# Optimization experiments

Measured on AMD Instinct MI355X. Metric: run time of the kernel, lower is better.

The kernel has to match this reference:

```python
import jax, jax.numpy as jnp
import numpy as np

B, M, H, NH = 64, 512, 1024, 8
HD = H // NH
EPS = 1e-5


def setup_inputs() -> dict:
    key = jax.random.key(0)
    ks = jax.random.split(key, 16)
    def n(k, shape, s=0.02):
        return jax.random.normal(k, shape, dtype=jnp.float32) * s
    z = lambda shape: jnp.zeros(shape, jnp.float32)
    return {
        "x": jax.random.normal(ks[0], (B, M, M), dtype=jnp.float32),
        # 1x1 Conv2d(1->H): weight [H,1,1,1] flattened to [H], plus bias [H]
        "conv_w": n(ks[1], (H,)), "conv_b": n(ks[2], (H,)),
        # MLP: Linear(M->H), ReLU, Linear(H->H); weights stored [in,out]
        "w1": n(ks[3], (M, H)), "b1": z((H,)),
        "w2": n(ks[4], (H, H)), "b2": z((H,)),
        "ln_g": jnp.ones((H,), jnp.float32), "ln_b": z((H,)),
        "wq": n(ks[5], (H, H)), "bq": z((H,)),
        "wk": n(ks[6], (H, H)), "bk": z((H,)),
        "wv": n(ks[7], (H, H)), "bv": z((H,)),
        "wo": n(ks[8], (H, H)), "bo": z((H,)),
        "wp": n(ks[9], (H, H)), "bp": z((H,)),
    }


def reference(x, conv_w, conv_b, w1, b1, w2, b2, ln_g, ln_b,
              wq, bq, wk, bk, wv, bv, wo, bo, wp, bp):
    # RegionConvolution: 1x1 conv over 1 input channel to H channels, then
    # mean over channels. Since mean_c(x*w_c + b_c) = x*mean(w) + mean(b),
    # compute the reduced affine form (identical math, no [B,H,M,M] temp).
    x = x + (x * conv_w.mean() + conv_b.mean())          # residual conv add, [B,M,M]
    # RegionEmbeddingMLP
    x_reg = jnp.maximum(x @ w1 + b1, 0.0) @ w2 + b2      # [B,M,H]
    # LayerNorm
    mu = x_reg.mean(-1, keepdims=True)
    var = ((x_reg - mu) ** 2).mean(-1, keepdims=True)
    x_norm = (x_reg - mu) / jnp.sqrt(var + EPS) * ln_g + ln_b
    # MHSA with multiplicative off-diagonal mask (diagonal scores zeroed)
    def heads(y):
        return y.reshape(B, M, NH, HD).transpose(0, 2, 1, 3)  # [B,NH,M,HD]
    q = heads(x_norm @ wq + bq)
    k = heads(x_norm @ wk + bk)
    v = heads(x_norm @ wv + bv)
    scores = jnp.einsum('bhqd,bhkd->bhqk', q, k) / jnp.sqrt(jnp.float32(HD))
    scores = scores * (1.0 - jnp.eye(M, dtype=scores.dtype))  # zero diagonal
    attn = jax.nn.softmax(scores, axis=-1)
    ctx = jnp.einsum('bhqk,bhkd->bhqd', attn, v)
    ctx = ctx.transpose(0, 2, 1, 3).reshape(B, M, H)
    attn_out = ctx @ wo + bo
    attn_out = attn_out @ wp + bp                        # output_proj
    return attn_out + x_reg                              # residual, [B,M,H]
```

## Files before the change

### kernel.cpp

```cpp
#include <hip/hip_runtime.h>
#include <hip/hip_fp16.h>
#include <cstdint>
#include <cstddef>

typedef _Float16 f16;
typedef _Float16 f16x8 __attribute__((ext_vector_type(8)));
typedef _Float16 f16x4 __attribute__((ext_vector_type(4)));
typedef _Float16 f16x2 __attribute__((ext_vector_type(2)));
typedef float f32x4 __attribute__((ext_vector_type(4)));
typedef unsigned int ui4 __attribute__((ext_vector_type(4)));

#define NB 64
#define SEQ 512
#define HDIM 1024
#define NHEAD 8
#define HD 128
#define MR (NB * SEQ)
#define QK_LD 2048

__device__ __forceinline__ void async_copy16(const f16* g, f16* l) {
  __builtin_amdgcn_global_load_lds(
      (__attribute__((address_space(1))) void*)(void*)const_cast<f16*>(g),
      (__attribute__((address_space(3))) void*)l, 16, 0, 0);
}


__global__ __launch_bounds__(256) void conv_reduce(
    const float* __restrict__ cw, const float* __restrict__ cb,
    float* __restrict__ out2) {
  int t = threadIdx.x;
  float a = 0.f, b = 0.f;
  for (int i = t; i < HDIM; i += 256) { a += cw[i]; b += cb[i]; }
  for (int m = 32; m >= 1; m >>= 1) { a += __shfl_xor(a, m); b += __shfl_xor(b, m); }
  __shared__ float sa[4], sb[4];
  if ((t & 63) == 0) { sa[t >> 6] = a; sb[t >> 6] = b; }
  __syncthreads();
  if (t == 0) {
    out2[0] = (sa[0] + sa[1] + sa[2] + sa[3]) * (1.f / HDIM);
    out2[1] = (sb[0] + sb[1] + sb[2] + sb[3]) * (1.f / HDIM);
  }
}

__global__ __launch_bounds__(256) void prep_x(
    const float* __restrict__ x, const float* __restrict__ cs,
    f16* __restrict__ xh) {
  size_t i = (size_t)blockIdx.x * 256 + threadIdx.x;
  float cw = 1.f + cs[0], cb = cs[1];
  float4 v = ((const float4*)x)[i];
  f16x4 o;
  o[0] = (f16)(v.x * cw + cb);
  o[1] = (f16)(v.y * cw + cb);
  o[2] = (f16)(v.z * cw + cb);
  o[3] = (f16)(v.w * cw + cb);
  ((f16x4*)xh)[i] = o;
}

__global__ __launch_bounds__(256) void concat_bias(
    const float* __restrict__ bq, const float* __restrict__ bk,
    const float* __restrict__ bv, float* __restrict__ dst) {
  int i = blockIdx.x * 256 + threadIdx.x;
  if (i < 1024) dst[i] = bq[i];
  else if (i < 2048) dst[i] = bk[i - 1024];
  else dst[i] = bv[i - 2048];
}

__global__ __launch_bounds__(256) void cast_f16(
    const float* __restrict__ src, f16* __restrict__ dst) {
  size_t i = (size_t)blockIdx.x * 256 + threadIdx.x;
  float4 v = ((const float4*)src)[i];
  f16x4 o;
  o[0] = (f16)v.x; o[1] = (f16)v.y; o[2] = (f16)v.z; o[3] = (f16)v.w;
  ((f16x4*)dst)[i] = o;
}

__global__ __launch_bounds__(256) void fuse_bias_p1(
    const float* __restrict__ bo, const float* __restrict__ wp,
    float* __restrict__ partial) {
  int n = blockIdx.x * 256 + threadIdx.x;
  int jc = blockIdx.y;
  float s = 0.f;
#pragma unroll 8
  for (int j = jc * 128; j < jc * 128 + 128; j++) s += bo[j] * wp[(size_t)j * 1024 + n];
  partial[(size_t)jc * 1024 + n] = s;
}

__global__ __launch_bounds__(256) void fuse_bias_p2(
    const float* __restrict__ partial, const float* __restrict__ bp,
    float* __restrict__ bp2) {
  int n = blockIdx.x * 256 + threadIdx.x;
  float s = bp[n];
#pragma unroll
  for (int jc = 0; jc < 8; jc++) s += partial[(size_t)jc * 1024 + n];
  bp2[n] = s;
}

__global__ __launch_bounds__(256) void transpose_cast(
    const float* __restrict__ src, f16* __restrict__ dst, int K, int N) {
  __shared__ float tile[32][33];
  int tx = threadIdx.x, ty = threadIdx.y;
  int n0 = blockIdx.x * 32, k0 = blockIdx.y * 32;
#pragma unroll
  for (int r = 0; r < 32; r += 8) tile[ty + r][tx] = src[(size_t)(k0 + ty + r) * N + n0 + tx];
  __syncthreads();
#pragma unroll
  for (int r = 0; r < 32; r += 8)
    dst[(size_t)(n0 + ty + r) * K + k0 + tx] = (f16)tile[tx][ty + r];
}

__global__ __launch_bounds__(256) void transpose_cast5(
    const float* s0, const float* s1, const float* s2, const float* s3, const float* s4,
    f16* d0, f16* d1, f16* d2, f16* d3, f16* d4) {
  const float* src; f16* dst;
  switch (blockIdx.z) {
    case 0: src = s0; dst = d0; break;
    case 1: src = s1; dst = d1; break;
    case 2: src = s2; dst = d2; break;
    case 3: src = s3; dst = d3; break;
    default: src = s4; dst = d4; break;
  }
  __shared__ float tile[32][33];
  int tx = threadIdx.x, ty = threadIdx.y;
  int n0 = blockIdx.x * 32, k0 = blockIdx.y * 32;
#pragma unroll
  for (int r = 0; r < 32; r += 8) tile[ty + r][tx] = src[(size_t)(k0 + ty + r) * 1024 + n0 + tx];
  __syncthreads();
#pragma unroll
  for (int r = 0; r < 32; r += 8)
    dst[(size_t)(n0 + ty + r) * 1024 + k0 + tx] = (f16)tile[tx][ty + r];
}

__global__ __launch_bounds__(256) void ln_kernel(
    const f16* __restrict__ xin, const float* __restrict__ g,
    const float* __restrict__ bta, f16* __restrict__ out) {
  int row = blockIdx.x;
  int t = threadIdx.x;
  f16x4 vh = ((const f16x4*)(xin + (size_t)row * HDIM))[t];
  float vx = (float)vh[0], vy = (float)vh[1], vz = (float)vh[2], vw = (float)vh[3];
  float s = vx + vy + vz + vw;
  float s2 = vx * vx + vy * vy + vz * vz + vw * vw;
  for (int m = 32; m >= 1; m >>= 1) { s += __shfl_xor(s, m); s2 += __shfl_xor(s2, m); }
  __shared__ float sa[4], sb[4];
  if ((t & 63) == 0) { sa[t >> 6] = s; sb[t >> 6] = s2; }
  __syncthreads();
  float S = sa[0] + sa[1] + sa[2] + sa[3];
  float S2 = sb[0] + sb[1] + sb[2] + sb[3];
  float mu = S * (1.f / HDIM);
  float var = S2 * (1.f / HDIM) - mu * mu;
  float inv = rsqrtf(var + 1e-5f);
  float4 gv = ((const float4*)g)[t];
  float4 bv = ((const float4*)bta)[t];
  f16x4 o;
  o[0] = (f16)((vx - mu) * inv * gv.x + bv.x);
  o[1] = (f16)((vy - mu) * inv * gv.y + bv.y);
  o[2] = (f16)((vz - mu) * inv * gv.z + bv.z);
  o[3] = (f16)((vw - mu) * inv * gv.w + bv.w);
  ((f16x4*)(out + (size_t)row * HDIM))[t] = o;
}

template <int EPI>
__global__ __launch_bounds__(512) void gemm_nt(
    const f16* __restrict__ A, const f16* __restrict__ BT,
    const float* __restrict__ bias, void* __restrict__ Cout, int N, int K,
    const f16* __restrict__ Xres, f16* __restrict__ vTout) {
  __shared__ __align__(16) f16 As[128 * 64];
  __shared__ __align__(16) f16 Bs[128 * 64];
  const int tid = threadIdx.x;
  const int wave = tid >> 6, lane = tid & 63;
  const int l15 = lane & 15, quad = lane >> 4;

  const int gn = N >> 7;
  const int gm = (int)gridDim.x / gn;
  const int pid = blockIdx.x;
  const int npg = 16 * gn;
  const int gid = pid / npg;
  const int rem = pid - gid * npg;
  const int grows = min(16, gm - gid * 16);
  const int bm = gid * 16 + rem % grows;
  const int bn = rem / grows;

  const int wm = wave >> 2, wn = wave & 3;

  f32x4 z4 = {0.f, 0.f, 0.f, 0.f};
  f32x4 acc[4][2];
#pragma unroll
  for (int i = 0; i < 4; i++)
#pragma unroll
    for (int j = 0; j < 2; j++) acc[i][j] = z4;

  const int srow = tid >> 3;
  const int c = ((tid & 7) - (srow & 7)) & 7;
  const f16* Ag = A + (size_t)(bm * 128 + srow) * K + c * 8;
  const f16* Bg = BT + (size_t)(bn * 128 + srow) * K + c * 8;
  f16* Al0 = As + tid * 8;
  f16* Al1 = As + 64 * 64 + tid * 8;
  f16* Bl0 = Bs + tid * 8;
  f16* Bl1 = Bs + 64 * 64 + tid * 8;
  const size_t kstep = (size_t)64 * K;

  const int r7 = l15 & 7;

  for (int k0 = 0; k0 < K; k0 += 64) {
    async_copy16(Ag, Al0);
    async_copy16(Ag + kstep, Al1);
    async_copy16(Bg, Bl0);
    async_copy16(Bg + kstep, Bl1);
    Ag += 64; Bg += 64;
    __syncthreads();
#pragma unroll
    for (int s = 0; s < 2; s++) {
      f16x8 af[4], bfr[2];
#pragma unroll
      for (int t = 0; t < 4; t++) {
        int phys = (s * 4 + quad + r7) & 7;
        af[t] = *(const f16x8*)&As[(wm * 64 + t * 16 + l15) * 64 + phys * 8];
      }
#pragma unroll
      for (int u = 0; u < 2; u++) {
        int phys = (s * 4 + quad + r7) & 7;
        bfr[u] = *(const f16x8*)&Bs[(wn * 32 + u * 16 + l15) * 64 + phys * 8];
      }
#pragma unroll
      for (int i = 0; i < 4; i++)
#pragma unroll
        for (int j = 0; j < 2; j++)
          acc[i][j] = __builtin_amdgcn_mfma_f32_16x16x32_f16(af[i], bfr[j], acc[i][j], 0, 0, 0);
    }
    __syncthreads();
  }

  float* Cf = (float*)Cout;
  f16* Ch = (f16*)Cout;
#pragma unroll
  for (int i = 0; i < 4; i++) {
    int r0 = bm * 128 + wm * 64 + i * 16 + quad * 4;
#pragma unroll
    for (int j = 0; j < 2; j++) {
      int c0 = bn * 128 + wn * 32 + j * 16;
      int cc = c0 + l15;
      float bv = (EPI == 4) ? 0.f : bias[cc];
      if (EPI == 6 && c0 >= 2048) {
        int hh = (cc - 2048) >> 7, d = (cc - 2048) & 127;
        int bb = r0 >> 9, ml = r0 & 511;
        f16x4 o;
#pragma unroll
        for (int reg = 0; reg < 4; reg++) o[reg] = (f16)(acc[i][j][reg] + bv);
        *(f16x4*)&vTout[((size_t)(bb * NHEAD + hh) * HD + d) * SEQ + ml] = o;
      } else {
#pragma unroll
        for (int reg = 0; reg < 4; reg++) {
          float v = acc[i][j][reg] + bv;
          if (EPI == 0)      Ch[(size_t)(r0 + reg) * N + cc] = (f16)fmaxf(v, 0.f);
          else if (EPI == 1) Ch[(size_t)(r0 + reg) * N + cc] = (f16)v;
          else if (EPI == 4) Ch[(size_t)(r0 + reg) * N + cc] = (f16)v;
          else if (EPI == 5) {
            size_t idx = (size_t)(r0 + reg) * N + cc;
            Cf[idx] = v + (float)Xres[idx];
          } else {
            Ch[(size_t)(r0 + reg) * QK_LD + cc] = (f16)v;
          }
        }
      }
    }
  }
}

__global__ __launch_bounds__(512) void attn_kernel(
    const f16* __restrict__ qkv, const f16* __restrict__ vT,
    f16* __restrict__ ctx) {
  const int tid = threadIdx.x;
  const int wave = tid >> 6, lane = tid & 63;
  const int l15 = lane & 15, quad = lane >> 4;
  const int bidx = blockIdx.x;
  const int qc = bidx >> 9;
  const int bh = bidx & 511;
  const int h = bh & 7, bb = bh >> 3;

  const f16* Qbase = qkv + (size_t)(bb * SEQ) * QK_LD + h * 128;
  const f16* Kbase = Qbase + 1024;
  const f16* VTbase = vT + (size_t)(bb * NHEAD + h) * HD * SEQ;

  __shared__ __align__(16) f16 Ks[2 * 64 * 128];
  __shared__ __align__(16) f16 VTs[2 * 128 * 64];

  const float scale = 0.08838834764831845f;
  const int qrow0 = qc * 256 + wave * 32;
  f16x8 qf[2][4];
#pragma unroll
  for (int tm = 0; tm < 2; tm++)
#pragma unroll
    for (int s = 0; s < 4; s++) {
      qf[tm][s] = *(const f16x8*)(Qbase + (size_t)(qrow0 + tm * 16 + l15) * QK_LD + s * 32 + quad * 8);
#pragma unroll
      for (int e = 0; e < 8; e++) qf[tm][s][e] *= (f16)scale;
    }

  f32x4 z4 = {0.f, 0.f, 0.f, 0.f};
  f32x4 O[2][8];
#pragma unroll
  for (int i = 0; i < 2; i++)
#pragma unroll
    for (int j = 0; j < 8; j++) O[i][j] = z4;
  float lrow[2] = {0.f, 0.f};

  const int kc = ((tid & 15) - ((tid >> 4) & 15)) & 15;
  const f16* Kg = Kbase + (size_t)(tid >> 4) * QK_LD + kc * 8;
  const int vc = ((tid & 7) - ((tid >> 3) & 7)) & 7;
  const f16* Vg = VTbase + (size_t)(tid >> 3) * SEQ + vc * 8;

  const int r7 = l15 & 7;
  const bool qodd = (quad & 1) != 0;

#define STAGE_KV_(BUF, KT) do {                                               \
    const int kr_ = (KT) * 64;                                                \
    _Pragma("unroll") for (int i_ = 0; i_ < 2; i_++)                          \
      async_copy16(Kg + (size_t)(kr_ + 32 * i_) * QK_LD,                      \
                   Ks + (BUF) * 8192 + tid * 8 + 4096 * i_);                  \
    _Pragma("unroll") for (int i_ = 0; i_ < 2; i_++)                          \
      async_copy16(Vg + (size_t)(64 * i_) * SEQ + kr_,                        \
                   VTs + (BUF) * 8192 + tid * 8 + 4096 * i_);                 \
  } while (0)

  asm volatile("s_waitcnt vmcnt(0)" ::: "memory");
  STAGE_KV_(0, 0);

  for (int kt = 0; kt < 8; kt++) {
    const int buf = kt & 1;
    const f16* Ksb = Ks + buf * 8192;
    const f16* VTsb = VTs + buf * 8192;
    const int krow0 = kt * 64;

    if (kt < 7) {
      STAGE_KV_(buf ^ 1, kt + 1);
      asm volatile("s_waitcnt vmcnt(4)" ::: "memory");
    } else {
      asm volatile("s_waitcnt vmcnt(0)" ::: "memory");
    }
    __builtin_amdgcn_s_barrier();

    f32x4 ST[4][2];
#pragma unroll
    for (int i = 0; i < 4; i++)
#pragma unroll
      for (int j = 0; j < 2; j++) ST[i][j] = z4;
#pragma unroll
    for (int s = 0; s < 4; s++) {
      f16x8 bfr[4];
#pragma unroll
      for (int tn = 0; tn < 4; tn++) {
        int phys = (s * 4 + quad + l15) & 15;
        bfr[tn] = *(const f16x8*)&Ksb[(tn * 16 + l15) * 128 + phys * 8];
      }
      __builtin_amdgcn_s_setprio(1);
#pragma unroll
      for (int tn = 0; tn < 4; tn++)
#pragma unroll
        for (int tm = 0; tm < 2; tm++)
          ST[tn][tm] = __builtin_amdgcn_mfma_f32_16x16x32_f16(bfr[tn], qf[tm][s], ST[tn][tm], 0, 0, 0);
      __builtin_amdgcn_s_setprio(0);
    }

    f16x8 pa[2][2];
#pragma unroll
    for (int tm = 0; tm < 2; tm++) {
      const int qg = qrow0 + tm * 16 + l15;
      float rs = 0.f;
      unsigned int H[4][2];
#pragma unroll
      for (int tn = 0; tn < 4; tn++) {
        float p[4];
#pragma unroll
        for (int reg = 0; reg < 4; reg++) {
          int kg = krow0 + tn * 16 + quad * 4 + reg;
          float v = (kg == qg) ? 1.f : __expf(ST[tn][tm][reg]);
          p[reg] = v;
          rs += v;
        }
        f16x2 h01 = {(f16)p[0], (f16)p[1]};
        f16x2 h23 = {(f16)p[2], (f16)p[3]};
        H[tn][0] = __builtin_bit_cast(unsigned int, h01);
        H[tn][1] = __builtin_bit_cast(unsigned int, h23);
      }
      rs += __shfl_xor(rs, 16);
      rs += __shfl_xor(rs, 32);
      lrow[tm] += rs;

#pragma unroll
      for (int ks = 0; ks < 2; ks++) {
        unsigned int a0 = H[ks * 2][0], a1 = H[ks * 2][1];
        unsigned int b0 = H[ks * 2 + 1][0], b1 = H[ks * 2 + 1][1];
        asm volatile("s_nop 1\n\tv_permlane32_swap_b32 %0, %1\n\ts_nop 1"
                     : "+v"(a0), "+v"(b0));
        asm volatile("s_nop 1\n\tv_permlane32_swap_b32 %0, %1\n\ts_nop 1"
                     : "+v"(a1), "+v"(b1));
        unsigned int c0 = (unsigned int)__shfl_xor((int)a0, 16);
        unsigned int c1 = (unsigned int)__shfl_xor((int)a1, 16);
        unsigned int d0 = (unsigned int)__shfl_xor((int)b0, 16);
        unsigned int d1 = (unsigned int)__shfl_xor((int)b1, 16);
        ui4 wv;
        wv[0] = qodd ? d0 : a0;
        wv[1] = qodd ? d1 : a1;
        wv[2] = qodd ? b0 : c0;
        wv[3] = qodd ? b1 : c1;
        pa[tm][ks] = __builtin_bit_cast(f16x8, wv);
      }
    }

#pragma unroll
    for (int ks = 0; ks < 2; ks++) {
      __builtin_amdgcn_s_setprio(1);
#pragma unroll
      for (int tn = 0; tn < 8; tn++) {
        int phys = (ks * 4 + quad + r7) & 7;
        f16x8 vb = *(const f16x8*)&VTsb[(tn * 16 + l15) * 64 + phys * 8];
#pragma unroll
        for (int tm = 0; tm < 2; tm++)
          O[tm][tn] = __builtin_amdgcn_mfma_f32_16x16x32_f16(pa[tm][ks], vb, O[tm][tn], 0, 0, 0);
      }
      __builtin_amdgcn_s_setprio(0);
    }
    __builtin_amdgcn_s_barrier();
  }
#undef STAGE_KV_

#pragma unroll
  for (int tm = 0; tm < 2; tm++)
#pragma unroll
    for (int reg = 0; reg < 4; reg++) {
      float lv = __shfl(lrow[tm], quad * 4 + reg);
      float inv = 1.f / lv;
      int row = bb * SEQ + qrow0 + tm * 16 + quad * 4 + reg;
#pragma unroll
      for (int tn = 0; tn < 8; tn++) {
        int col = h * 128 + tn * 16 + l15;
        ctx[(size_t)row * HDIM + col] = (f16)(O[tm][tn][reg] * inv);
      }
    }
}


extern "C" void kernel_launch(void* const* d_in, const int* in_sizes, int n_in,
                              void* d_out, int out_size, void* d_ws, size_t ws_size,
                              hipStream_t stream) {
  (void)in_sizes; (void)n_in; (void)out_size; (void)ws_size;
  const float* x      = (const float*)d_in[0];
  const float* conv_w = (const float*)d_in[1];
  const float* conv_b = (const float*)d_in[2];
  const float* w1     = (const float*)d_in[3];
  const float* b1     = (const float*)d_in[4];
  const float* w2     = (const float*)d_in[5];
  const float* b2     = (const float*)d_in[6];
  const float* ln_g   = (const float*)d_in[7];
  const float* ln_b   = (const float*)d_in[8];
  const float* wq     = (const float*)d_in[9];
  const float* bq     = (const float*)d_in[10];
  const float* wk     = (const float*)d_in[11];
  const float* bk     = (const float*)d_in[12];
  const float* wv     = (const float*)d_in[13];
  const float* bv     = (const float*)d_in[14];
  const float* wo     = (const float*)d_in[15];
  const float* bo     = (const float*)d_in[16];
  const float* wp     = (const float*)d_in[17];
  const float* bp     = (const float*)d_in[18];
  float* out = (float*)d_out;

  char* ws = (char*)d_ws;
  size_t off = 0;
  auto alloc = [&](size_t bytes) {
    char* p = ws + off;
    off += (bytes + 255) & ~(size_t)255;
    return p;
  };
  float* cs    = (float*)alloc(8);
  f16* w1T     = (f16*)alloc((size_t)1024 * 512 * 2);
  f16* w2T     = (f16*)alloc((size_t)1024 * 1024 * 2);
  f16* qkvT    = (f16*)alloc((size_t)3072 * 1024 * 2);
  f16* wpT     = (f16*)alloc((size_t)1024 * 1024 * 2);
  f16* woh     = (f16*)alloc((size_t)1024 * 1024 * 2);
  f16* woPT    = (f16*)alloc((size_t)1024 * 1024 * 2);
  float* bqkv  = (float*)alloc((size_t)3072 * 4);
  float* bp2   = (float*)alloc((size_t)1024 * 4);
  float* part  = (float*)alloc((size_t)8 * 1024 * 4);
  f16* qkvQK   = (f16*)alloc((size_t)MR * QK_LD * 2);
  f16* h1      = (f16*)alloc((size_t)MR * 1024 * 2);
  f16* x_norm  = (f16*)alloc((size_t)MR * 1024 * 2);
  f16* x_regh  = (f16*)alloc((size_t)MR * 1024 * 2);
  f16* xh = qkvQK;
  f16* vT = h1;
  f16* ctx = x_norm;

  dim3 tb(32, 8);
  conv_reduce<<<1, 256, 0, stream>>>(conv_w, conv_b, cs);
  transpose_cast<<<dim3(32, 16), tb, 0, stream>>>(w1, w1T, 512, 1024);
  transpose_cast5<<<dim3(32, 32, 5), tb, 0, stream>>>(
      w2, wq, wk, wv, wp,
      w2T, qkvT, qkvT + (size_t)1024 * 1024, qkvT + (size_t)2048 * 1024, wpT);
  cast_f16<<<1024, 256, 0, stream>>>(wo, woh);
  concat_bias<<<12, 256, 0, stream>>>(bq, bk, bv, bqkv);
  fuse_bias_p1<<<dim3(4, 8), 256, 0, stream>>>(bo, wp, part);
  fuse_bias_p2<<<4, 256, 0, stream>>>(part, bp, bp2);
  prep_x<<<16384, 256, 0, stream>>>(x, cs, xh);

  gemm_nt<4><<<dim3(64), 512, 0, stream>>>(wpT, woh, nullptr, (void*)woPT, 1024, 1024, nullptr, nullptr);

  gemm_nt<0><<<dim3(256 * 8), 512, 0, stream>>>(xh, w1T, b1, (void*)h1, 1024, 512, nullptr, nullptr);
  gemm_nt<1><<<dim3(256 * 8), 512, 0, stream>>>(h1, w2T, b2, (void*)x_regh, 1024, 1024, nullptr, nullptr);
  ln_kernel<<<32768, 256, 0, stream>>>(x_regh, ln_g, ln_b, x_norm);
  gemm_nt<6><<<dim3(256 * 24), 512, 0, stream>>>(x_norm, qkvT, bqkv, (void*)qkvQK, 3072, 1024, nullptr, vT);
  attn_kernel<<<1024, 512, 0, stream>>>(qkvQK, vT, ctx);
  gemm_nt<5><<<dim3(256 * 8), 512, 0, stream>>>(ctx, woPT, bp2, (void*)out, 1024, 1024, x_regh, nullptr);
}
```

Measured before the change: 853.9 us.

## Fold LayerNorm into QKV GEMM epilogue and merge prep kernels

LayerNorm is split: a small kernel computes per-row mean and inverse std, and the gamma scaling is folded into the QKV weights. The beta and mean corrections are applied through precomputed column sums in the QKV GEMM epilogue, so the GEMM reads the raw f16 x_reg directly. This removes the writing and re-reading of the normalized activation tensor. The many small weight and bias prep kernels are merged into two multi-role launches to cut launch overhead. In exchange, the GEMM runs on un-normalized f16 inputs, which can cost precision, and the epilogue does extra per-row loads.

```diff
diff --git a/kernel.cpp b/kernel.cpp
--- a/kernel.cpp
+++ b/kernel.cpp
@@ -24,114 +24,139 @@
       (__attribute__((address_space(3))) void*)l, 16, 0, 0);
 }
 
-
-__global__ __launch_bounds__(256) void conv_reduce(
-    const float* __restrict__ cw, const float* __restrict__ cb,
-    float* __restrict__ out2) {
-  int t = threadIdx.x;
-  float a = 0.f, b = 0.f;
-  for (int i = t; i < HDIM; i += 256) { a += cw[i]; b += cb[i]; }
-  for (int m = 32; m >= 1; m >>= 1) { a += __shfl_xor(a, m); b += __shfl_xor(b, m); }
+__global__ __launch_bounds__(256) void prep1(
+    const float* __restrict__ cw, const float* __restrict__ cb, float* __restrict__ cs,
+    const float* __restrict__ w1, f16* __restrict__ w1T,
+    const float* __restrict__ w2, const float* __restrict__ wq,
+    const float* __restrict__ wk, const float* __restrict__ wv,
+    const float* __restrict__ wp,
+    f16* __restrict__ w2T, f16* __restrict__ qkvT, f16* __restrict__ wpT,
+    const float* __restrict__ wo, f16* __restrict__ woh,
+    const float* __restrict__ bq, const float* __restrict__ bk,
+    const float* __restrict__ bv, float* __restrict__ bqkv,
+    const float* __restrict__ bo, float* __restrict__ part,
+    const float* __restrict__ g, const float* __restrict__ lb,
+    float2* __restrict__ cpart) {
+  __shared__ float tile[32][33];
   __shared__ float sa[4], sb[4];
-  if ((t & 63) == 0) { sa[t >> 6] = a; sb[t >> 6] = b; }
-  __syncthreads();
-  if (t == 0) {
-    out2[0] = (sa[0] + sa[1] + sa[2] + sa[3]) * (1.f / HDIM);
-    out2[1] = (sb[0] + sb[1] + sb[2] + sb[3]) * (1.f / HDIM);
+  const int b = blockIdx.x;
+  const int tid = threadIdx.x;
+
+  if (b == 0) {
+    float a = 0.f, bb = 0.f;
+    for (int i = tid; i < HDIM; i += 256) { a += cw[i]; bb += cb[i]; }
+    for (int m = 32; m >= 1; m >>= 1) { a += __shfl_xor(a, m); bb += __shfl_xor(bb, m); }
+    if ((tid & 63) == 0) { sa[tid >> 6] = a; sb[tid >> 6] = bb; }
+    __syncthreads();
+    if (tid == 0) {
+      cs[0] = (sa[0] + sa[1] + sa[2] + sa[3]) * (1.f / HDIM);
+      cs[1] = (sb[0] + sb[1] + sb[2] + sb[3]) * (1.f / HDIM);
+    }
+  } else if (b < 513) {
+    int idx = b - 1;
+    int bx = idx & 31, by = idx >> 5;
+    int tx = tid & 31, ty = tid >> 5;
+    int n0 = bx * 32, k0 = by * 32;
+#pragma unroll
+    for (int r = 0; r < 32; r += 8) tile[ty + r][tx] = w1[(size_t)(k0 + ty + r) * 1024 + n0 + tx];
+    __syncthreads();
+#pragma unroll
+    for (int r = 0; r < 32; r += 8)
+      w1T[(size_t)(n0 + ty + r) * 512 + k0 + tx] = (f16)tile[tx][ty + r];
+  } else if (b < 5633) {
+    int idx = b - 513;
+    int z = idx >> 10, rem = idx & 1023;
+    int bx = rem & 31, by = rem >> 5;
+    const float* src; f16* dst; bool sc = false;
+    switch (z) {
+      case 0: src = w2; dst = w2T; break;
+      case 1: src = wq; dst = qkvT; sc = true; break;
+      case 2: src = wk; dst = qkvT + (size_t)1024 * 1024; sc = true; break;
+      case 3: src = wv; dst = qkvT + (size_t)2048 * 1024; sc = true; break;
+      default: src = wp; dst = wpT; break;
+    }
+    int tx = tid & 31, ty = tid >> 5;
+    int n0 = bx * 32, k0 = by * 32;
+#pragma unroll
+    for (int r = 0; r < 32; r += 8) tile[ty + r][tx] = src[(size_t)(k0 + ty + r) * 1024 + n0 + tx];
+    __syncthreads();
+    float gk = sc ? g[k0 + tx] : 1.f;
+#pragma unroll
+    for (int r = 0; r < 32; r += 8)
+      dst[(size_t)(n0 + ty + r) * 1024 + k0 + tx] = (f16)(tile[tx][ty + r] * gk);
+  } else if (b < 6657) {
+    size_t i = (size_t)(b - 5633) * 256 + tid;
+    float4 v = ((const float4*)wo)[i];
+    f16x4 o;
+    o[0] = (f16)v.x; o[1] = (f16)v.y; o[2] = (f16)v.z; o[3] = (f16)v.w;
+    ((f16x4*)woh)[i] = o;
+  } else if (b < 6669) {
+    int i = (b - 6657) * 256 + tid;
+    if (i < 1024) bqkv[i] = bq[i];
+    else if (i < 2048) bqkv[i] = bk[i - 1024];
+    else bqkv[i] = bv[i - 2048];
+  } else if (b < 6701) {
+    int idx = b - 6669;
+    int nb = idx & 3, jc = idx >> 2;
+    int n = nb * 256 + tid;
+    float s = 0.f;
+#pragma unroll 8
+    for (int j = jc * 128; j < jc * 128 + 128; j++) s += bo[j] * wp[(size_t)j * 1024 + n];
+    part[(size_t)jc * 1024 + n] = s;
+  } else {
+    int idx = b - 6701;
+    int nb = idx % 12, jc = idx / 12;
+    int n = nb * 256 + tid;
+    int sel = n >> 10, col = n & 1023;
+    const float* W = (sel == 0) ? wq : (sel == 1) ? wk : wv;
+    float s1 = 0.f, s2 = 0.f;
+#pragma unroll 4
+    for (int k = jc * 128; k < jc * 128 + 128; k++) {
+      float w = W[(size_t)k * 1024 + col];
+      s1 += g[k] * w;
+      s2 += lb[k] * w;
+    }
+    cpart[(size_t)jc * 3072 + n] = make_float2(s1, s2);
   }
 }
 
-__global__ __launch_bounds__(256) void prep_x(
-    const float* __restrict__ x, const float* __restrict__ cs,
-    f16* __restrict__ xh) {
-  size_t i = (size_t)blockIdx.x * 256 + threadIdx.x;
-  float cw = 1.f + cs[0], cb = cs[1];
-  float4 v = ((const float4*)x)[i];
-  f16x4 o;
-  o[0] = (f16)(v.x * cw + cb);
-  o[1] = (f16)(v.y * cw + cb);
-  o[2] = (f16)(v.z * cw + cb);
-  o[3] = (f16)(v.w * cw + cb);
-  ((f16x4*)xh)[i] = o;
-}
-
-__global__ __launch_bounds__(256) void concat_bias(
-    const float* __restrict__ bq, const float* __restrict__ bk,
-    const float* __restrict__ bv, float* __restrict__ dst) {
-  int i = blockIdx.x * 256 + threadIdx.x;
-  if (i < 1024) dst[i] = bq[i];
-  else if (i < 2048) dst[i] = bk[i - 1024];
-  else dst[i] = bv[i - 2048];
-}
-
-__global__ __launch_bounds__(256) void cast_f16(
-    const float* __restrict__ src, f16* __restrict__ dst) {
-  size_t i = (size_t)blockIdx.x * 256 + threadIdx.x;
-  float4 v = ((const float4*)src)[i];
-  f16x4 o;
-  o[0] = (f16)v.x; o[1] = (f16)v.y; o[2] = (f16)v.z; o[3] = (f16)v.w;
-  ((f16x4*)dst)[i] = o;
-}
-
-__global__ __launch_bounds__(256) void fuse_bias_p1(
-    const float* __restrict__ bo, const float* __restrict__ wp,
-    float* __restrict__ partial) {
-  int n = blockIdx.x * 256 + threadIdx.x;
-  int jc = blockIdx.y;
-  float s = 0.f;
-#pragma unroll 8
-  for (int j = jc * 128; j < jc * 128 + 128; j++) s += bo[j] * wp[(size_t)j * 1024 + n];
-  partial[(size_t)jc * 1024 + n] = s;
-}
-
-__global__ __launch_bounds__(256) void fuse_bias_p2(
-    const float* __restrict__ partial, const float* __restrict__ bp,
-    float* __restrict__ bp2) {
-  int n = blockIdx.x * 256 + threadIdx.x;
-  float s = bp[n];
-#pragma unroll
-  for (int jc = 0; jc < 8; jc++) s += partial[(size_t)jc * 1024 + n];
-  bp2[n] = s;
-}
-
-__global__ __launch_bounds__(256) void transpose_cast(
-    const float* __restrict__ src, f16* __restrict__ dst, int K, int N) {
-  __shared__ float tile[32][33];
-  int tx = threadIdx.x, ty = threadIdx.y;
-  int n0 = blockIdx.x * 32, k0 = blockIdx.y * 32;
-#pragma unroll
-  for (int r = 0; r < 32; r += 8) tile[ty + r][tx] = src[(size_t)(k0 + ty + r) * N + n0 + tx];
-  __syncthreads();
-#pragma unroll
-  for (int r = 0; r < 32; r += 8)
-    dst[(size_t)(n0 + ty + r) * K + k0 + tx] = (f16)tile[tx][ty + r];
-}
-
-__global__ __launch_bounds__(256) void transpose_cast5(
-    const float* s0, const float* s1, const float* s2, const float* s3, const float* s4,
-    f16* d0, f16* d1, f16* d2, f16* d3, f16* d4) {
-  const float* src; f16* dst;
-  switch (blockIdx.z) {
-    case 0: src = s0; dst = d0; break;
-    case 1: src = s1; dst = d1; break;
-    case 2: src = s2; dst = d2; break;
-    case 3: src = s3; dst = d3; break;
-    default: src = s4; dst = d4; break;
+__global__ __launch_bounds__(256) void prep2(
+    const float* __restrict__ x, const float* __restrict__ cs, f16* __restrict__ xh,
+    const float* __restrict__ part, const float* __restrict__ bp, float* __restrict__ bp2,
+    const float2* __restrict__ cpart, const float* __restrict__ bqkv,
+    float2* __restrict__ c12) {
+  const int b = blockIdx.x;
+  const int tid = threadIdx.x;
+  if (b < 16384) {
+    size_t i = (size_t)b * 256 + tid;
+    float cwv = 1.f + cs[0], cbv = cs[1];
+    float4 v = ((const float4*)x)[i];
+    f16x4 o;
+    o[0] = (f16)(v.x * cwv + cbv);
+    o[1] = (f16)(v.y * cwv + cbv);
+    o[2] = (f16)(v.z * cwv + cbv);
+    o[3] = (f16)(v.w * cwv + cbv);
+    ((f16x4*)xh)[i] = o;
+  } else if (b < 16388) {
+    int n = (b - 16384) * 256 + tid;
+    float s = bp[n];
+#pragma unroll
+    for (int jc = 0; jc < 8; jc++) s += part[(size_t)jc * 1024 + n];
+    bp2[n] = s;
+  } else {
+    int n = (b - 16388) * 256 + tid;
+    float s1 = 0.f, s2 = 0.f;
+#pragma unroll
+    for (int jc = 0; jc < 8; jc++) {
+      float2 p = cpart[(size_t)jc * 3072 + n];
+      s1 += p.x; s2 += p.y;
+    }
+    c12[n] = make_float2(s1, s2 + bqkv[n]);
   }
-  __shared__ float tile[32][33];
-  int tx = threadIdx.x, ty = threadIdx.y;
-  int n0 = blockIdx.x * 32, k0 = blockIdx.y * 32;
-#pragma unroll
-  for (int r = 0; r < 32; r += 8) tile[ty + r][tx] = src[(size_t)(k0 + ty + r) * 1024 + n0 + tx];
-  __syncthreads();
-#pragma unroll
-  for (int r = 0; r < 32; r += 8)
-    dst[(size_t)(n0 + ty + r) * 1024 + k0 + tx] = (f16)tile[tx][ty + r];
-}
-
-__global__ __launch_bounds__(256) void ln_kernel(
-    const f16* __restrict__ xin, const float* __restrict__ g,
-    const float* __restrict__ bta, f16* __restrict__ out) {
+}
+
+__global__ __launch_bounds__(256) void ln_stats(
+    const f16* __restrict__ xin, float2* __restrict__ stats) {
   int row = blockIdx.x;
   int t = threadIdx.x;
   f16x4 vh = ((const f16x4*)(xin + (size_t)row * HDIM))[t];
@@ -142,26 +167,21 @@
   __shared__ float sa[4], sb[4];
   if ((t & 63) == 0) { sa[t >> 6] = s; sb[t >> 6] = s2; }
   __syncthreads();
-  float S = sa[0] + sa[1] + sa[2] + sa[3];
-  float S2 = sb[0] + sb[1] + sb[2] + sb[3];
-  float mu = S * (1.f / HDIM);
-  float var = S2 * (1.f / HDIM) - mu * mu;
-  float inv = rsqrtf(var + 1e-5f);
-  float4 gv = ((const float4*)g)[t];
-  float4 bv = ((const float4*)bta)[t];
-  f16x4 o;
-  o[0] = (f16)((vx - mu) * inv * gv.x + bv.x);
-  o[1] = (f16)((vy - mu) * inv * gv.y + bv.y);
-  o[2] = (f16)((vz - mu) * inv * gv.z + bv.z);
-  o[3] = (f16)((vw - mu) * inv * gv.w + bv.w);
-  ((f16x4*)(out + (size_t)row * HDIM))[t] = o;
+  if (t == 0) {
+    float S = sa[0] + sa[1] + sa[2] + sa[3];
+    float S2 = sb[0] + sb[1] + sb[2] + sb[3];
+    float mu = S * (1.f / HDIM);
+    float var = S2 * (1.f / HDIM) - mu * mu;
+    stats[row] = make_float2(mu, rsqrtf(var + 1e-5f));
+  }
 }
 
 template <int EPI>
 __global__ __launch_bounds__(512) void gemm_nt(
     const f16* __restrict__ A, const f16* __restrict__ BT,
     const float* __restrict__ bias, void* __restrict__ Cout, int N, int K,
-    const f16* __restrict__ Xres, f16* __restrict__ vTout) {
+    const f16* __restrict__ Xres, f16* __restrict__ vTout,
+    const float2* __restrict__ c12, const float2* __restrict__ stats) {
   __shared__ __align__(16) f16 As[128 * 64];
   __shared__ __align__(16) f16 Bs[128 * 64];
   const int tid = threadIdx.x;
@@ -233,22 +253,36 @@
 #pragma unroll
   for (int i = 0; i < 4; i++) {
     int r0 = bm * 128 + wm * 64 + i * 16 + quad * 4;
+    float av[4], bf2[4];
+    if (EPI == 6) {
+#pragma unroll
+      for (int reg = 0; reg < 4; reg++) {
+        float2 st = stats[r0 + reg];
+        av[reg] = st.y;
+        bf2[reg] = -st.y * st.x;
+      }
+    }
 #pragma unroll
     for (int j = 0; j < 2; j++) {
       int c0 = bn * 128 + wn * 32 + j * 16;
       int cc = c0 + l15;
-      float bv = (EPI == 4) ? 0.f : bias[cc];
+      float bv = (EPI == 4 || EPI == 6) ? 0.f : bias[cc];
+      float2 cv;
+      if (EPI == 6) cv = c12[cc];
       if (EPI == 6 && c0 >= 2048) {
         int hh = (cc - 2048) >> 7, d = (cc - 2048) & 127;
         int bb = r0 >> 9, ml = r0 & 511;
         f16x4 o;
 #pragma unroll
-        for (int reg = 0; reg < 4; reg++) o[reg] = (f16)(acc[i][j][reg] + bv);
+        for (int reg = 0; reg < 4; reg++)
+          o[reg] = (f16)(av[reg] * acc[i][j][reg] + bf2[reg] * cv.x + cv.y);
         *(f16x4*)&vTout[((size_t)(bb * NHEAD + hh) * HD + d) * SEQ + ml] = o;
       } else {
 #pragma unroll
         for (int reg = 0; reg < 4; reg++) {
-          float v = acc[i][j][reg] + bv;
+          float v;
+          if (EPI == 6) v = av[reg] * acc[i][j][reg] + bf2[reg] * cv.x + cv.y;
+          else          v = acc[i][j][reg] + bv;
           if (EPI == 0)      Ch[(size_t)(r0 + reg) * N + cc] = (f16)fmaxf(v, 0.f);
           else if (EPI == 1) Ch[(size_t)(r0 + reg) * N + cc] = (f16)v;
           else if (EPI == 4) Ch[(size_t)(r0 + reg) * N + cc] = (f16)v;
@@ -480,6 +514,9 @@
   float* bqkv  = (float*)alloc((size_t)3072 * 4);
   float* bp2   = (float*)alloc((size_t)1024 * 4);
   float* part  = (float*)alloc((size_t)8 * 1024 * 4);
+  float2* cpart = (float2*)alloc((size_t)8 * 3072 * 8);
+  float2* c12   = (float2*)alloc((size_t)3072 * 8);
+  float2* stats = (float2*)alloc((size_t)MR * 8);
   f16* qkvQK   = (f16*)alloc((size_t)MR * QK_LD * 2);
   f16* h1      = (f16*)alloc((size_t)MR * 1024 * 2);
   f16* x_norm  = (f16*)alloc((size_t)MR * 1024 * 2);
@@ -488,24 +525,22 @@
   f16* vT = h1;
   f16* ctx = x_norm;
 
-  dim3 tb(32, 8);
-  conv_reduce<<<1, 256, 0, stream>>>(conv_w, conv_b, cs);
-  transpose_cast<<<dim3(32, 16), tb, 0, stream>>>(w1, w1T, 512, 1024);
-  transpose_cast5<<<dim3(32, 32, 5), tb, 0, stream>>>(
-      w2, wq, wk, wv, wp,
-      w2T, qkvT, qkvT + (size_t)1024 * 1024, qkvT + (size_t)2048 * 1024, wpT);
-  cast_f16<<<1024, 256, 0, stream>>>(wo, woh);
-  concat_bias<<<12, 256, 0, stream>>>(bq, bk, bv, bqkv);
-  fuse_bias_p1<<<dim3(4, 8), 256, 0, stream>>>(bo, wp, part);
-  fuse_bias_p2<<<4, 256, 0, stream>>>(part, bp, bp2);
-  prep_x<<<16384, 256, 0, stream>>>(x, cs, xh);
-
-  gemm_nt<4><<<dim3(64), 512, 0, stream>>>(wpT, woh, nullptr, (void*)woPT, 1024, 1024, nullptr, nullptr);
-
-  gemm_nt<0><<<dim3(256 * 8), 512, 0, stream>>>(xh, w1T, b1, (void*)h1, 1024, 512, nullptr, nullptr);
-  gemm_nt<1><<<dim3(256 * 8), 512, 0, stream>>>(h1, w2T, b2, (void*)x_regh, 1024, 1024, nullptr, nullptr);
-  ln_kernel<<<32768, 256, 0, stream>>>(x_regh, ln_g, ln_b, x_norm);
-  gemm_nt<6><<<dim3(256 * 24), 512, 0, stream>>>(x_norm, qkvT, bqkv, (void*)qkvQK, 3072, 1024, nullptr, vT);
+  prep1<<<6797, 256, 0, stream>>>(
+      conv_w, conv_b, cs, w1, w1T, w2, wq, wk, wv, wp, w2T, qkvT, wpT,
+      wo, woh, bq, bk, bv, bqkv, bo, part, ln_g, ln_b, cpart);
+  prep2<<<16400, 256, 0, stream>>>(x, cs, xh, part, bp, bp2, cpart, bqkv, c12);
+
+  gemm_nt<4><<<dim3(64), 512, 0, stream>>>(wpT, woh, nullptr, (void*)woPT, 1024, 1024,
+                                           nullptr, nullptr, nullptr, nullptr);
+
+  gemm_nt<0><<<dim3(256 * 8), 512, 0, stream>>>(xh, w1T, b1, (void*)h1, 1024, 512,
+                                                nullptr, nullptr, nullptr, nullptr);
+  gemm_nt<1><<<dim3(256 * 8), 512, 0, stream>>>(h1, w2T, b2, (void*)x_regh, 1024, 1024,
+                                                nullptr, nullptr, nullptr, nullptr);
+  ln_stats<<<32768, 256, 0, stream>>>(x_regh, stats);
+  gemm_nt<6><<<dim3(256 * 24), 512, 0, stream>>>(x_regh, qkvT, nullptr, (void*)qkvQK, 3072, 1024,
+                                                 nullptr, vT, c12, stats);
   attn_kernel<<<1024, 512, 0, stream>>>(qkvQK, vT, ctx);
-  gemm_nt<5><<<dim3(256 * 8), 512, 0, stream>>>(ctx, woPT, bp2, (void*)out, 1024, 1024, x_regh, nullptr);
-}
+  gemm_nt<5><<<dim3(256 * 8), 512, 0, stream>>>(ctx, woPT, bp2, (void*)out, 1024, 1024,
+                                                x_regh, nullptr, nullptr, nullptr);
+}
```

New measurement: 873.5 us. 1.02x slower.
